# Kernel tuning notes

Hardware: AMD Instinct MI355X
Metric: run time of the kernel (lower is better)

The kernel has to match this reference:

```python
import jax, jax.numpy as jnp
import numpy as np

T, B, D_IN, UNITS = 2000, 32, 512, 1024
P_KEEP = 0.8      # eval-mode dropout mask value (1 - 0.2) for 'in', 'recur', 'orig'
BN_EPS = 1e-5     # torch BatchNorm1d default eps


def setup_inputs() -> dict:
    key = jax.random.key(0)
    ks = jax.random.split(key, 6)
    s_in = 1.0 / np.sqrt(D_IN)
    s_h = 1.0 / np.sqrt(UNITS)
    # orthogonal init for recurrent mats (as in ligru_orthinit)
    uh = jnp.linalg.qr(jax.random.normal(ks[2], (UNITS, UNITS)))[0].astype(jnp.float32)
    uz = jnp.linalg.qr(jax.random.normal(ks[3], (UNITS, UNITS)))[0].astype(jnp.float32)
    return {
        "x": jax.random.normal(ks[0], (T, B, D_IN), dtype=jnp.float32),
        "Wh": jax.random.uniform(ks[1], (UNITS, D_IN), jnp.float32, -s_in, s_in),
        "Wz": jax.random.uniform(ks[4], (UNITS, D_IN), jnp.float32, -s_in, s_in),
        "Uh": uh,
        "Uz": uz,
        "gamma_wh": jnp.ones((UNITS,), jnp.float32),
        "beta_wh": jnp.zeros((UNITS,), jnp.float32),
        "gamma_wz": jnp.ones((UNITS,), jnp.float32),
        "beta_wz": jnp.zeros((UNITS,), jnp.float32),
    }


def _batchnorm(y, gamma, beta):
    # BatchNorm1d over flattened (T*B, UNITS), biased variance (training-style stats)
    yf = y.reshape(-1, y.shape[-1])
    mean = yf.mean(axis=0)
    var = yf.var(axis=0)
    return (y - mean) * jax.lax.rsqrt(var + BN_EPS) * gamma + beta


def reference(x, Wh, Wz, Uh, Uz, gamma_wh, beta_wh, gamma_wz, beta_wz):
    # input dropout (eval mode -> constant scale 0.8) then linear, no bias (BN on)
    xd = x * P_KEEP
    wh_out = _batchnorm(jnp.einsum("tbd,ud->tbu", xd, Wh), gamma_wh, beta_wh)
    wz_out = _batchnorm(jnp.einsum("tbd,ud->tbu", xd, Wz), gamma_wz, beta_wz)

    h0 = jnp.zeros((x.shape[1], Wh.shape[0]), x.dtype)

    def step(h, inp):
        whk, wzk = inp
        z = jax.nn.sigmoid(wzk + (h * P_KEEP) @ Uz.T)   # update gate
        a = whk + (h * P_KEEP) @ Uh.T                   # candidate pre-activation
        hcand = jax.nn.relu(a) * P_KEEP                 # 'orig' dropout scale
        h_new = z * h + (1.0 - z) * hcand
        return h_new, h_new

    _, hs = jax.lax.scan(step, h0, (wh_out, wz_out))    # hs: [T, B, UNITS]
    return hs
```

## Files before the change

### kernel.cpp

```cpp
#include <hip/hip_runtime.h>


#define T_STEPS 2000
#define NCOLS   2048
#define PKEEP   0.8f
#define BN_EPSF 1e-5f
#define NW      256

typedef __attribute__((ext_vector_type(8))) short bf16x8;
typedef __attribute__((ext_vector_type(4))) float f32x4;
typedef __attribute__((ext_vector_type(4))) unsigned int u32x4;

static __device__ __forceinline__ unsigned short f2bf(float f) {
  unsigned u = __builtin_bit_cast(unsigned, f);
  unsigned r = u + 0x7FFFu + ((u >> 16) & 1u);
  return (unsigned short)(r >> 16);
}
static __device__ __forceinline__ float bf2f(unsigned short s) {
  unsigned u = ((unsigned)s) << 16;
  return __builtin_bit_cast(float, u);
}

__global__ void k_convw(const float* __restrict__ Wh, const float* __restrict__ Wz,
                        unsigned short* __restrict__ Wb) {
  int i = blockIdx.x * 256 + threadIdx.x;
  int e = i * 4;
  int n = e >> 9;
  int k = e & 511;
  const float* src = (n < 1024) ? (Wh + (size_t)n * 512 + k)
                                : (Wz + (size_t)(n - 1024) * 512 + k);
  float4 v = *(const float4*)src;
  *(ushort4*)(Wb + e) = make_ushort4(f2bf(v.x), f2bf(v.y), f2bf(v.z), f2bf(v.w));
}

__global__ __launch_bounds__(256, 2) void k_gemm(
    const float* __restrict__ X, const unsigned short* __restrict__ Wb,
    unsigned short* __restrict__ P, float* __restrict__ sums, float* __restrict__ sumsq) {
  __shared__ __align__(16) unsigned short As[128 * 32];
  __shared__ __align__(16) unsigned short Bs[128 * 32];
  const int tid  = threadIdx.x;
  const int bm   = blockIdx.x >> 4, bn = blockIdx.x & 15;
  const int lane = tid & 63, wid = tid >> 6;
  const int wm   = wid >> 1, wn = wid & 1;
  const int lrow = lane & 15, lk = lane >> 4;

  f32x4 acc[4][4] = {};

  for (int kk = 0; kk < 512; kk += 32) {
    __syncthreads();
#pragma unroll
    for (int j = 0; j < 2; ++j) {
      int c = j * 256 + wid * 64 + lane;
      int brow = c >> 2, b8 = (c & 3) * 8;
      const unsigned short* gp = Wb + (size_t)(bn * 128 + brow) * 512 + kk + b8;
      __builtin_amdgcn_global_load_lds(
          (const __attribute__((address_space(1))) unsigned int*)gp,
          (__attribute__((address_space(3))) unsigned int*)(Bs + (size_t)(j * 256 + wid * 64) * 8),
          16, 0, 0);
    }
    {
      int arow = tid >> 1, ahalf = tid & 1;
      const float4* xp = (const float4*)(X + (size_t)(bm * 128 + arow) * 512 + kk + ahalf * 16);
      unsigned v[8];
#pragma unroll
      for (int j = 0; j < 4; ++j) {
        float4 f = xp[j];
        v[j * 2 + 0] = (unsigned)f2bf(f.x) | ((unsigned)f2bf(f.y) << 16);
        v[j * 2 + 1] = (unsigned)f2bf(f.z) | ((unsigned)f2bf(f.w) << 16);
      }
      u32x4* ap = (u32x4*)(As + arow * 32 + ahalf * 16);
      u32x4 t0 = {v[0], v[1], v[2], v[3]};
      u32x4 t1 = {v[4], v[5], v[6], v[7]};
      ap[0] = t0; ap[1] = t1;
    }
    __syncthreads();

    bf16x8 af[4], bfr[4];
#pragma unroll
    for (int mt = 0; mt < 4; ++mt)
      af[mt] = *(const bf16x8*)(As + (wm * 64 + mt * 16 + lrow) * 32 + lk * 8);
#pragma unroll
    for (int nt = 0; nt < 4; ++nt)
      bfr[nt] = *(const bf16x8*)(Bs + (wn * 64 + nt * 16 + lrow) * 32 + lk * 8);
#pragma unroll
    for (int mt = 0; mt < 4; ++mt)
#pragma unroll
      for (int nt = 0; nt < 4; ++nt)
        acc[mt][nt] = __builtin_amdgcn_mfma_f32_16x16x32_bf16(af[mt], bfr[nt], acc[mt][nt], 0, 0, 0);
  }

#pragma unroll
  for (int mt = 0; mt < 4; ++mt)
#pragma unroll
    for (int nt = 0; nt < 4; ++nt) {
      f32x4 a = acc[mt][nt];
      int gcol  = bn * 128 + wn * 64 + nt * 16 + lrow;
      int grow0 = bm * 128 + wm * 64 + mt * 16 + lk * 4;
#pragma unroll
      for (int rr = 0; rr < 4; ++rr)
        P[(size_t)(grow0 + rr) * NCOLS + gcol] = f2bf(a[rr]);
    }
#pragma unroll
  for (int nt = 0; nt < 4; ++nt) {
    float s = 0.f, q = 0.f;
#pragma unroll
    for (int mt = 0; mt < 4; ++mt) {
      f32x4 a = acc[mt][nt];
#pragma unroll
      for (int rr = 0; rr < 4; ++rr) { s += a[rr]; q += a[rr] * a[rr]; }
    }
    s += __shfl_xor(s, 16); s += __shfl_xor(s, 32);
    q += __shfl_xor(q, 16); q += __shfl_xor(q, 32);
    if (lane < 16) {
      int gcol = bn * 128 + wn * 64 + nt * 16 + lrow;
      atomicAdd(&sums[gcol], s);
      atomicAdd(&sumsq[gcol], q);
    }
  }
}

__global__ __launch_bounds__(256, 1) void k_scan(
    const float* __restrict__ Uh, const float* __restrict__ Uz,
    const float* __restrict__ gwh, const float* __restrict__ bwh,
    const float* __restrict__ gwz, const float* __restrict__ bwz,
    const unsigned short* P,
    const float* __restrict__ sums, const float* __restrict__ sumsq,
    unsigned long long* hrec,
    unsigned int* ctrl,
    float* out)
{
  __shared__ __align__(16) unsigned char hlds[16384];

  const int tid  = threadIdx.x;
  const int lane = tid & 63;
  const int wid  = tid >> 6;
  const int lrow = lane & 15, lk = lane >> 4;

  const int g    = blockIdx.x & 7;
  const int role = blockIdx.x >> 3;
  const int b0   = g * 4;
  const int u0w  = role * 32 + wid * 8;
  const bool isH = (lrow >= 8);
  const int unit = u0w + (lrow & 7);
  const int col  = isH ? unit : (1024 + unit);

  float scl, bia;
  {
    float s = sums[col], q = sumsq[col];
    float gam = isH ? gwh[unit] : gwz[unit];
    float bet = isH ? bwh[unit] : bwz[unit];
    float mean = s * (1.0f / 64000.0f);
    float var  = q * (1.0f / 64000.0f) - mean * mean;
    float rstd = rsqrtf(var + BN_EPSF);
    scl = gam * rstd;
    bia = bet - mean * scl;
  }

  const float* urow = (isH ? Uh : Uz) + (size_t)unit * 1024;
  bf16x8 bfrag[32];
#pragma unroll
  for (int kt = 0; kt < 32; ++kt) {
    const float4* p4 = (const float4*)(urow + kt * 32 + lk * 8);
    float4 fa = p4[0], fb = p4[1];
    bf16x8 tv;
    tv[0] = (short)f2bf(fa.x * PKEEP); tv[1] = (short)f2bf(fa.y * PKEEP);
    tv[2] = (short)f2bf(fa.z * PKEEP); tv[3] = (short)f2bf(fa.w * PKEEP);
    tv[4] = (short)f2bf(fb.x * PKEEP); tv[5] = (short)f2bf(fb.y * PKEEP);
    tv[6] = (short)f2bf(fb.z * PKEEP); tv[7] = (short)f2bf(fb.w * PKEEP);
    bfrag[kt] = tv;
  }

  unsigned short pf[4], pn1[4];
#pragma unroll
  for (int rr = 0; rr < 4; ++rr) {
    pf[rr]  = P[(size_t)(b0 + rr) * NCOLS + col];
    pn1[rr] = P[(size_t)(32 + b0 + rr) * NCOLS + col];
  }
  __syncthreads();

  if (tid == 0) {
    __hip_atomic_fetch_add(&ctrl[0], 1u, __ATOMIC_RELEASE, __HIP_MEMORY_SCOPE_SYSTEM);
    while (__hip_atomic_load(&ctrl[0], __ATOMIC_RELAXED, __HIP_MEMORY_SCOPE_SYSTEM) < NW)
      __builtin_amdgcn_s_sleep(8);
  }
  __syncthreads();

  f32x4 hown = {0.f, 0.f, 0.f, 0.f};

  for (int t = 0; t < T_STEPS; ++t) {
    const int par = t & 1;

    const unsigned long long* rb = hrec + (((size_t)(g * 2 + par)) << 11) + tid;
    unsigned long long rec[8];
#pragma unroll
    for (int j = 0; j < 8; ++j)
      rec[j] = __hip_atomic_load(rb + 256 * j, __ATOMIC_RELAXED, __HIP_MEMORY_SCOPE_SYSTEM);
    while (true) {
      unsigned bad = 0;
#pragma unroll
      for (int j = 0; j < 8; ++j)
        if ((unsigned)(rec[j] >> 32) < (unsigned)t) bad |= (1u << j);
      if (!bad) break;
      __builtin_amdgcn_s_sleep(1);
#pragma unroll
      for (int j = 0; j < 8; ++j)
        if (bad & (1u << j))
          rec[j] = __hip_atomic_load(rb + 256 * j, __ATOMIC_RELAXED, __HIP_MEMORY_SCOPE_SYSTEM);
    }
    asm volatile("s_waitcnt vmcnt(0)" ::: "memory");

    unsigned short pn2[4] = {0, 0, 0, 0};
    if (t + 2 < T_STEPS) {
#pragma unroll
      for (int rr = 0; rr < 4; ++rr)
        pn2[rr] = P[(size_t)((t + 2) * 32 + b0 + rr) * NCOLS + col];
    }

    unsigned char* hb = hlds + par * 8192;
#pragma unroll
    for (int j = 0; j < 8; ++j) {
      int idx = tid + 256 * j;
      int row = idx >> 9, up = idx & 511;
      int byteoff = (row * 2048 + up * 4) ^ ((row & 3) << 5);
      *(unsigned*)(hb + byteoff) = (unsigned)rec[j];
    }
    asm volatile("s_waitcnt lgkmcnt(0)" ::: "memory");
    __builtin_amdgcn_sched_barrier(0);
    __builtin_amdgcn_s_barrier();
    __builtin_amdgcn_sched_barrier(0);

    f32x4 ac0 = {0.f, 0.f, 0.f, 0.f}, ac1 = ac0, ac2 = ac0, ac3 = ac0;
#pragma unroll
    for (int kt = 0; kt < 32; ++kt) {
      int ab = ((lane & 3) * 2048 + kt * 64 + lk * 16) ^ ((lane & 3) << 5);
      bf16x8 af = *(const bf16x8*)(hb + ab);
      if ((kt & 3) == 0)      ac0 = __builtin_amdgcn_mfma_f32_16x16x32_bf16(af, bfrag[kt], ac0, 0, 0, 0);
      else if ((kt & 3) == 1) ac1 = __builtin_amdgcn_mfma_f32_16x16x32_bf16(af, bfrag[kt], ac1, 0, 0, 0);
      else if ((kt & 3) == 2) ac2 = __builtin_amdgcn_mfma_f32_16x16x32_bf16(af, bfrag[kt], ac2, 0, 0, 0);
      else                    ac3 = __builtin_amdgcn_mfma_f32_16x16x32_bf16(af, bfrag[kt], ac3, 0, 0, 0);
    }
    f32x4 dsum = (ac0 + ac1) + (ac2 + ac3);

    float pre[4], oth[4];
#pragma unroll
    for (int rr = 0; rr < 4; ++rr) {
      pre[rr] = dsum[rr] + bf2f(pf[rr]) * scl + bia;
      oth[rr] = __shfl_xor(pre[rr], 8);
    }

    if (lk == 0 && isH) {
      float hn[4];
#pragma unroll
      for (int rr = 0; rr < 4; ++rr) {
        float zz = 1.0f / (1.0f + __expf(-oth[rr]));
        float hc = fmaxf(pre[rr], 0.0f) * PKEEP;
        hn[rr] = zz * hown[rr] + (1.0f - zz) * hc;
        hown[rr] = hn[rr];
      }
      float pp[4];
#pragma unroll
      for (int rr = 0; rr < 4; ++rr) pp[rr] = __shfl_xor(hn[rr], 1);
      if ((lane & 1) == 0) {
        unsigned long long* hbn = hrec + (((size_t)(g * 2 + ((t + 1) & 1))) << 11)
                                + (unit >> 1);
        unsigned tagw = (unsigned)(t + 1);
#pragma unroll
        for (int rr = 0; rr < 4; ++rr) {
          unsigned long long rcd = ((unsigned long long)tagw << 32)
                                 | (unsigned)f2bf(hn[rr]) | ((unsigned)f2bf(pp[rr]) << 16);
          __hip_atomic_store(hbn + rr * 512, rcd,
                             __ATOMIC_RELAXED, __HIP_MEMORY_SCOPE_SYSTEM);
        }
#pragma unroll
        for (int rr = 0; rr < 4; ++rr) {
          float2 ov = {hn[rr], pp[rr]};
          *(float2*)(out + (size_t)(t * 32 + b0 + rr) * 1024 + unit) = ov;
        }
      }
    }

#pragma unroll
    for (int rr = 0; rr < 4; ++rr) { pf[rr] = pn1[rr]; pn1[rr] = pn2[rr]; }
  }
}

extern "C" void kernel_launch(void* const* d_in, const int* in_sizes, int n_in,
                              void* d_out, int out_size, void* d_ws, size_t ws_size,
                              hipStream_t stream) {
  (void)in_sizes; (void)n_in; (void)out_size; (void)ws_size;
  const float* x   = (const float*)d_in[0];
  const float* Wh  = (const float*)d_in[1];
  const float* Wz  = (const float*)d_in[2];
  const float* Uh  = (const float*)d_in[3];
  const float* Uz  = (const float*)d_in[4];
  const float* gwh = (const float*)d_in[5];
  const float* bwh = (const float*)d_in[6];
  const float* gwz = (const float*)d_in[7];
  const float* bwz = (const float*)d_in[8];

  char* ws = (char*)d_ws;
  float*              sums  = (float*)(ws + 0);
  float*              sumsq = (float*)(ws + 8192);
  unsigned long long* hrec  = (unsigned long long*)(ws + 16384);
  unsigned int*       ctrl  = (unsigned int*)(ws + 278528);
  unsigned short*     Wb    = (unsigned short*)(ws + 278784);

  hipMemsetAsync(d_ws, 0, 278784, stream);
  k_convw<<<1024, 256, 0, stream>>>(Wh, Wz, Wb);
  k_gemm<<<8000, 256, 0, stream>>>(x, Wb, (unsigned short*)d_out, sums, sumsq);
  k_scan<<<NW, 256, 0, stream>>>(Uh, Uz, gwh, bwh, gwz, bwz,
                                 (const unsigned short*)d_out, sums, sumsq,
                                 hrec, ctrl, (float*)d_out);
}
```

Measured before the change: 7.818 ms.

## Halve scan workgroups to 512 threads and add per-wave tag flags for step sync

The persistent scan kernel now runs as 128 workgroups of 512 threads instead of 256 of 256, so each workgroup covers 64 units per batch group. Cross-workgroup readiness is now checked through a small per-wave tag array: one wave polls 128 tags and the workgroup barriers before loading the tagged h records. Each wave publishes its tag after its stores drain. The goal is to cut the number of polling agents and the contention on the global h records each step. The cost is an extra barrier and tag round-trip per step, plus more register pressure from the 512-thread launch bounds.

Result: slower. 8.926 ms (+14.2%).

```diff
diff --git a/kernel.cpp b/kernel.cpp
--- a/kernel.cpp
+++ b/kernel.cpp
@@ -5,7 +5,7 @@
 #define NCOLS   2048
 #define PKEEP   0.8f
 #define BN_EPSF 1e-5f
-#define NW      256
+#define NWG     128
 
 typedef __attribute__((ext_vector_type(8))) short bf16x8;
 typedef __attribute__((ext_vector_type(4))) float f32x4;
@@ -119,13 +119,14 @@
   }
 }
 
-__global__ __launch_bounds__(256, 1) void k_scan(
+__global__ __launch_bounds__(512, 2) void k_scan(
     const float* __restrict__ Uh, const float* __restrict__ Uz,
     const float* __restrict__ gwh, const float* __restrict__ bwh,
     const float* __restrict__ gwz, const float* __restrict__ bwz,
     const unsigned short* P,
     const float* __restrict__ sums, const float* __restrict__ sumsq,
     unsigned long long* hrec,
+    unsigned int* tags,
     unsigned int* ctrl,
     float* out)
 {
@@ -139,7 +140,7 @@
   const int g    = blockIdx.x & 7;
   const int role = blockIdx.x >> 3;
   const int b0   = g * 4;
-  const int u0w  = role * 32 + wid * 8;
+  const int u0w  = role * 64 + wid * 8;
   const bool isH = (lrow >= 8);
   const int unit = u0w + (lrow & 7);
   const int col  = isH ? unit : (1024 + unit);
@@ -180,7 +181,7 @@
 
   if (tid == 0) {
     __hip_atomic_fetch_add(&ctrl[0], 1u, __ATOMIC_RELEASE, __HIP_MEMORY_SCOPE_SYSTEM);
-    while (__hip_atomic_load(&ctrl[0], __ATOMIC_RELAXED, __HIP_MEMORY_SCOPE_SYSTEM) < NW)
+    while (__hip_atomic_load(&ctrl[0], __ATOMIC_RELAXED, __HIP_MEMORY_SCOPE_SYSTEM) < NWG)
       __builtin_amdgcn_s_sleep(8);
   }
   __syncthreads();
@@ -190,36 +191,51 @@
   for (int t = 0; t < T_STEPS; ++t) {
     const int par = t & 1;
 
+    unsigned short pn2[4] = {0, 0, 0, 0};
+    if (t + 2 < T_STEPS) {
+#pragma unroll
+      for (int rr = 0; rr < 4; ++rr)
+        pn2[rr] = P[(size_t)((t + 2) * 32 + b0 + rr) * NCOLS + col];
+    }
+
+    if (wid == 0) {
+      const unsigned* tg = tags + (((size_t)(g * 2 + par)) << 7);
+      unsigned ta = __hip_atomic_load(tg + lane, __ATOMIC_RELAXED, __HIP_MEMORY_SCOPE_SYSTEM);
+      unsigned tb = __hip_atomic_load(tg + 64 + lane, __ATOMIC_RELAXED, __HIP_MEMORY_SCOPE_SYSTEM);
+      while (!__all((ta >= (unsigned)t) && (tb >= (unsigned)t))) {
+        __builtin_amdgcn_s_sleep(1);
+        if (ta < (unsigned)t)
+          ta = __hip_atomic_load(tg + lane, __ATOMIC_RELAXED, __HIP_MEMORY_SCOPE_SYSTEM);
+        if (tb < (unsigned)t)
+          tb = __hip_atomic_load(tg + 64 + lane, __ATOMIC_RELAXED, __HIP_MEMORY_SCOPE_SYSTEM);
+      }
+    }
+    asm volatile("" ::: "memory");
+    __builtin_amdgcn_s_barrier();
+    asm volatile("" ::: "memory");
+
     const unsigned long long* rb = hrec + (((size_t)(g * 2 + par)) << 11) + tid;
-    unsigned long long rec[8];
-#pragma unroll
-    for (int j = 0; j < 8; ++j)
-      rec[j] = __hip_atomic_load(rb + 256 * j, __ATOMIC_RELAXED, __HIP_MEMORY_SCOPE_SYSTEM);
+    unsigned long long rec[4];
+#pragma unroll
+    for (int j = 0; j < 4; ++j)
+      rec[j] = __hip_atomic_load(rb + 512 * j, __ATOMIC_RELAXED, __HIP_MEMORY_SCOPE_SYSTEM);
     while (true) {
       unsigned bad = 0;
 #pragma unroll
-      for (int j = 0; j < 8; ++j)
+      for (int j = 0; j < 4; ++j)
         if ((unsigned)(rec[j] >> 32) < (unsigned)t) bad |= (1u << j);
       if (!bad) break;
       __builtin_amdgcn_s_sleep(1);
 #pragma unroll
-      for (int j = 0; j < 8; ++j)
+      for (int j = 0; j < 4; ++j)
         if (bad & (1u << j))
-          rec[j] = __hip_atomic_load(rb + 256 * j, __ATOMIC_RELAXED, __HIP_MEMORY_SCOPE_SYSTEM);
-    }
-    asm volatile("s_waitcnt vmcnt(0)" ::: "memory");
-
-    unsigned short pn2[4] = {0, 0, 0, 0};
-    if (t + 2 < T_STEPS) {
-#pragma unroll
-      for (int rr = 0; rr < 4; ++rr)
-        pn2[rr] = P[(size_t)((t + 2) * 32 + b0 + rr) * NCOLS + col];
+          rec[j] = __hip_atomic_load(rb + 512 * j, __ATOMIC_RELAXED, __HIP_MEMORY_SCOPE_SYSTEM);
     }
 
     unsigned char* hb = hlds + par * 8192;
 #pragma unroll
-    for (int j = 0; j < 8; ++j) {
-      int idx = tid + 256 * j;
+    for (int j = 0; j < 4; ++j) {
+      int idx = tid + 512 * j;
       int row = idx >> 9, up = idx & 511;
       int byteoff = (row * 2048 + up * 4) ^ ((row & 3) << 5);
       *(unsigned*)(hb + byteoff) = (unsigned)rec[j];
@@ -277,6 +293,13 @@
           *(float2*)(out + (size_t)(t * 32 + b0 + rr) * 1024 + unit) = ov;
         }
       }
+    }
+
+    asm volatile("s_waitcnt vmcnt(0)" ::: "memory");
+    __builtin_amdgcn_sched_barrier(0);
+    if (lane == 8) {
+      __hip_atomic_store(tags + (((size_t)(g * 2 + ((t + 1) & 1))) << 7) + (role * 8 + wid),
+                         (unsigned)(t + 1), __ATOMIC_RELAXED, __HIP_MEMORY_SCOPE_SYSTEM);
     }
 
 #pragma unroll
@@ -302,13 +325,14 @@
   float*              sums  = (float*)(ws + 0);
   float*              sumsq = (float*)(ws + 8192);
   unsigned long long* hrec  = (unsigned long long*)(ws + 16384);
-  unsigned int*       ctrl  = (unsigned int*)(ws + 278528);
-  unsigned short*     Wb    = (unsigned short*)(ws + 278784);
-
-  hipMemsetAsync(d_ws, 0, 278784, stream);
+  unsigned int*       tags  = (unsigned int*)(ws + 278528);
+  unsigned int*       ctrl  = (unsigned int*)(ws + 286720);
+  unsigned short*     Wb    = (unsigned short*)(ws + 286848);
+
+  hipMemsetAsync(d_ws, 0, 286848, stream);
   k_convw<<<1024, 256, 0, stream>>>(Wh, Wz, Wb);
   k_gemm<<<8000, 256, 0, stream>>>(x, Wb, (unsigned short*)d_out, sums, sumsq);
-  k_scan<<<NW, 256, 0, stream>>>(Uh, Uz, gwh, bwh, gwz, bwz,
-                                 (const unsigned short*)d_out, sums, sumsq,
-                                 hrec, ctrl, (float*)d_out);
-}
+  k_scan<<<NWG, 512, 0, stream>>>(Uh, Uz, gwh, bwh, gwz, bwz,
+                                  (const unsigned short*)d_out, sums, sumsq,
+                                  hrec, tags, ctrl, (float*)d_out);
+}
```

## Halve scan workgroups, each interleaving two batch groups to overlap sync waits

Applied to the files above, without the earlier changes.

The recurrent scan kernel now launches 128 workgroups instead of 256. Each one keeps the same U weight fragments in registers and processes two batch groups per time step. Group B's hidden-state records are loaded and polled while group A's MFMA and gate math run, so some of the cross-workgroup synchronization latency is hidden behind compute. The cost is twice the serial compute per workgroup per step and half the CUs left idle.

Measured after the change: 8.031 ms. 1.03x slower.

```diff
diff --git a/kernel.cpp b/kernel.cpp
--- a/kernel.cpp
+++ b/kernel.cpp
@@ -5,7 +5,7 @@
 #define NCOLS   2048
 #define PKEEP   0.8f
 #define BN_EPSF 1e-5f
-#define NW      256
+#define NWG     128
 
 typedef __attribute__((ext_vector_type(8))) short bf16x8;
 typedef __attribute__((ext_vector_type(4))) float f32x4;
@@ -129,16 +129,17 @@
     unsigned int* ctrl,
     float* out)
 {
-  __shared__ __align__(16) unsigned char hlds[16384];
+  __shared__ __align__(16) unsigned char hlds[4][8192];
 
   const int tid  = threadIdx.x;
   const int lane = tid & 63;
   const int wid  = tid >> 6;
   const int lrow = lane & 15, lk = lane >> 4;
 
-  const int g    = blockIdx.x & 7;
-  const int role = blockIdx.x >> 3;
-  const int b0   = g * 4;
+  const int pair = blockIdx.x & 3;
+  const int role = blockIdx.x >> 2;
+  const int gA   = pair * 2, gB = pair * 2 + 1;
+  const int b0A  = gA * 4,   b0B = gB * 4;
   const int u0w  = role * 32 + wid * 8;
   const bool isH = (lrow >= 8);
   const int unit = u0w + (lrow & 7);
@@ -170,117 +171,213 @@
     bfrag[kt] = tv;
   }
 
-  unsigned short pf[4], pn1[4];
+  unsigned short pfA[4], pn1A[4], pfB[4], pn1B[4];
 #pragma unroll
   for (int rr = 0; rr < 4; ++rr) {
-    pf[rr]  = P[(size_t)(b0 + rr) * NCOLS + col];
-    pn1[rr] = P[(size_t)(32 + b0 + rr) * NCOLS + col];
+    pfA[rr]  = P[(size_t)(b0A + rr) * NCOLS + col];
+    pn1A[rr] = P[(size_t)(32 + b0A + rr) * NCOLS + col];
+    pfB[rr]  = P[(size_t)(b0B + rr) * NCOLS + col];
+    pn1B[rr] = P[(size_t)(32 + b0B + rr) * NCOLS + col];
   }
   __syncthreads();
 
   if (tid == 0) {
     __hip_atomic_fetch_add(&ctrl[0], 1u, __ATOMIC_RELEASE, __HIP_MEMORY_SCOPE_SYSTEM);
-    while (__hip_atomic_load(&ctrl[0], __ATOMIC_RELAXED, __HIP_MEMORY_SCOPE_SYSTEM) < NW)
+    while (__hip_atomic_load(&ctrl[0], __ATOMIC_RELAXED, __HIP_MEMORY_SCOPE_SYSTEM) < NWG)
       __builtin_amdgcn_s_sleep(8);
   }
   __syncthreads();
 
-  f32x4 hown = {0.f, 0.f, 0.f, 0.f};
+  float hownA[4] = {0.f, 0.f, 0.f, 0.f};
+  float hownB[4] = {0.f, 0.f, 0.f, 0.f};
 
   for (int t = 0; t < T_STEPS; ++t) {
-    const int par = t & 1;
-
-    const unsigned long long* rb = hrec + (((size_t)(g * 2 + par)) << 11) + tid;
-    unsigned long long rec[8];
+    const int par  = t & 1;
+    const int npar = (t + 1) & 1;
+    const unsigned tagw = (unsigned)(t + 1);
+
+    const unsigned long long* rbA = hrec + (((size_t)(gA * 2 + par)) << 11) + tid;
+    unsigned long long recA[8];
 #pragma unroll
     for (int j = 0; j < 8; ++j)
-      rec[j] = __hip_atomic_load(rb + 256 * j, __ATOMIC_RELAXED, __HIP_MEMORY_SCOPE_SYSTEM);
+      recA[j] = __hip_atomic_load(rbA + 256 * j, __ATOMIC_RELAXED, __HIP_MEMORY_SCOPE_SYSTEM);
     while (true) {
       unsigned bad = 0;
 #pragma unroll
       for (int j = 0; j < 8; ++j)
-        if ((unsigned)(rec[j] >> 32) < (unsigned)t) bad |= (1u << j);
+        if ((unsigned)(recA[j] >> 32) < (unsigned)t) bad |= (1u << j);
       if (!bad) break;
       __builtin_amdgcn_s_sleep(1);
 #pragma unroll
       for (int j = 0; j < 8; ++j)
         if (bad & (1u << j))
-          rec[j] = __hip_atomic_load(rb + 256 * j, __ATOMIC_RELAXED, __HIP_MEMORY_SCOPE_SYSTEM);
+          recA[j] = __hip_atomic_load(rbA + 256 * j, __ATOMIC_RELAXED, __HIP_MEMORY_SCOPE_SYSTEM);
     }
     asm volatile("s_waitcnt vmcnt(0)" ::: "memory");
 
-    unsigned short pn2[4] = {0, 0, 0, 0};
+    unsigned short pn2A[4] = {0, 0, 0, 0}, pn2B[4] = {0, 0, 0, 0};
     if (t + 2 < T_STEPS) {
 #pragma unroll
-      for (int rr = 0; rr < 4; ++rr)
-        pn2[rr] = P[(size_t)((t + 2) * 32 + b0 + rr) * NCOLS + col];
-    }
-
-    unsigned char* hb = hlds + par * 8192;
-#pragma unroll
-    for (int j = 0; j < 8; ++j) {
-      int idx = tid + 256 * j;
-      int row = idx >> 9, up = idx & 511;
-      int byteoff = (row * 2048 + up * 4) ^ ((row & 3) << 5);
-      *(unsigned*)(hb + byteoff) = (unsigned)rec[j];
+      for (int rr = 0; rr < 4; ++rr) {
+        pn2A[rr] = P[(size_t)((t + 2) * 32 + b0A + rr) * NCOLS + col];
+        pn2B[rr] = P[(size_t)((t + 2) * 32 + b0B + rr) * NCOLS + col];
+      }
+    }
+
+    {
+      unsigned char* hb = hlds[par];
+#pragma unroll
+      for (int j = 0; j < 8; ++j) {
+        int idx = tid + 256 * j;
+        int row = idx >> 9, up = idx & 511;
+        int byteoff = (row * 2048 + up * 4) ^ ((row & 3) << 5);
+        *(unsigned*)(hb + byteoff) = (unsigned)recA[j];
+      }
     }
     asm volatile("s_waitcnt lgkmcnt(0)" ::: "memory");
     __builtin_amdgcn_sched_barrier(0);
     __builtin_amdgcn_s_barrier();
     __builtin_amdgcn_sched_barrier(0);
 
-    f32x4 ac0 = {0.f, 0.f, 0.f, 0.f}, ac1 = ac0, ac2 = ac0, ac3 = ac0;
-#pragma unroll
-    for (int kt = 0; kt < 32; ++kt) {
-      int ab = ((lane & 3) * 2048 + kt * 64 + lk * 16) ^ ((lane & 3) << 5);
-      bf16x8 af = *(const bf16x8*)(hb + ab);
-      if ((kt & 3) == 0)      ac0 = __builtin_amdgcn_mfma_f32_16x16x32_bf16(af, bfrag[kt], ac0, 0, 0, 0);
-      else if ((kt & 3) == 1) ac1 = __builtin_amdgcn_mfma_f32_16x16x32_bf16(af, bfrag[kt], ac1, 0, 0, 0);
-      else if ((kt & 3) == 2) ac2 = __builtin_amdgcn_mfma_f32_16x16x32_bf16(af, bfrag[kt], ac2, 0, 0, 0);
-      else                    ac3 = __builtin_amdgcn_mfma_f32_16x16x32_bf16(af, bfrag[kt], ac3, 0, 0, 0);
-    }
-    f32x4 dsum = (ac0 + ac1) + (ac2 + ac3);
-
-    float pre[4], oth[4];
+    const unsigned long long* rbB = hrec + (((size_t)(gB * 2 + par)) << 11) + tid;
+    unsigned long long recB[8];
+#pragma unroll
+    for (int j = 0; j < 8; ++j)
+      recB[j] = __hip_atomic_load(rbB + 256 * j, __ATOMIC_RELAXED, __HIP_MEMORY_SCOPE_SYSTEM);
+
+    {
+      unsigned char* hb = hlds[par];
+      f32x4 ac0 = {0.f, 0.f, 0.f, 0.f}, ac1 = ac0, ac2 = ac0, ac3 = ac0;
+#pragma unroll
+      for (int kt = 0; kt < 32; ++kt) {
+        int ab = ((lane & 3) * 2048 + kt * 64 + lk * 16) ^ ((lane & 3) << 5);
+        bf16x8 af = *(const bf16x8*)(hb + ab);
+        if ((kt & 3) == 0)      ac0 = __builtin_amdgcn_mfma_f32_16x16x32_bf16(af, bfrag[kt], ac0, 0, 0, 0);
+        else if ((kt & 3) == 1) ac1 = __builtin_amdgcn_mfma_f32_16x16x32_bf16(af, bfrag[kt], ac1, 0, 0, 0);
+        else if ((kt & 3) == 2) ac2 = __builtin_amdgcn_mfma_f32_16x16x32_bf16(af, bfrag[kt], ac2, 0, 0, 0);
+        else                    ac3 = __builtin_amdgcn_mfma_f32_16x16x32_bf16(af, bfrag[kt], ac3, 0, 0, 0);
+      }
+      f32x4 dsum = (ac0 + ac1) + (ac2 + ac3);
+
+      float pre[4], oth[4];
+#pragma unroll
+      for (int rr = 0; rr < 4; ++rr) {
+        pre[rr] = dsum[rr] + bf2f(pfA[rr]) * scl + bia;
+        oth[rr] = __shfl_xor(pre[rr], 8);
+      }
+      if (lk == 0 && isH) {
+        float hn[4];
+#pragma unroll
+        for (int rr = 0; rr < 4; ++rr) {
+          float zz = 1.0f / (1.0f + __expf(-oth[rr]));
+          float hc = fmaxf(pre[rr], 0.0f) * PKEEP;
+          hn[rr] = zz * hownA[rr] + (1.0f - zz) * hc;
+          hownA[rr] = hn[rr];
+        }
+        float pp[4];
+#pragma unroll
+        for (int rr = 0; rr < 4; ++rr) pp[rr] = __shfl_xor(hn[rr], 1);
+        if ((lane & 1) == 0) {
+          unsigned long long* hbn = hrec + (((size_t)(gA * 2 + npar)) << 11) + (unit >> 1);
+#pragma unroll
+          for (int rr = 0; rr < 4; ++rr) {
+            unsigned long long rcd = ((unsigned long long)tagw << 32)
+                                   | (unsigned)f2bf(hn[rr]) | ((unsigned)f2bf(pp[rr]) << 16);
+            __hip_atomic_store(hbn + rr * 512, rcd,
+                               __ATOMIC_RELAXED, __HIP_MEMORY_SCOPE_SYSTEM);
+          }
+#pragma unroll
+          for (int rr = 0; rr < 4; ++rr) {
+            float2 ov = {hn[rr], pp[rr]};
+            *(float2*)(out + (size_t)(t * 32 + b0A + rr) * 1024 + unit) = ov;
+          }
+        }
+      }
+    }
+
+    while (true) {
+      unsigned bad = 0;
+#pragma unroll
+      for (int j = 0; j < 8; ++j)
+        if ((unsigned)(recB[j] >> 32) < (unsigned)t) bad |= (1u << j);
+      if (!bad) break;
+      __builtin_amdgcn_s_sleep(1);
+#pragma unroll
+      for (int j = 0; j < 8; ++j)
+        if (bad & (1u << j))
+          recB[j] = __hip_atomic_load(rbB + 256 * j, __ATOMIC_RELAXED, __HIP_MEMORY_SCOPE_SYSTEM);
+    }
+
+    {
+      unsigned char* hb = hlds[2 + par];
+#pragma unroll
+      for (int j = 0; j < 8; ++j) {
+        int idx = tid + 256 * j;
+        int row = idx >> 9, up = idx & 511;
+        int byteoff = (row * 2048 + up * 4) ^ ((row & 3) << 5);
+        *(unsigned*)(hb + byteoff) = (unsigned)recB[j];
+      }
+    }
+    asm volatile("s_waitcnt lgkmcnt(0)" ::: "memory");
+    __builtin_amdgcn_sched_barrier(0);
+    __builtin_amdgcn_s_barrier();
+    __builtin_amdgcn_sched_barrier(0);
+
+    {
+      unsigned char* hb = hlds[2 + par];
+      f32x4 ac0 = {0.f, 0.f, 0.f, 0.f}, ac1 = ac0, ac2 = ac0, ac3 = ac0;
+#pragma unroll
+      for (int kt = 0; kt < 32; ++kt) {
+        int ab = ((lane & 3) * 2048 + kt * 64 + lk * 16) ^ ((lane & 3) << 5);
+        bf16x8 af = *(const bf16x8*)(hb + ab);
+        if ((kt & 3) == 0)      ac0 = __builtin_amdgcn_mfma_f32_16x16x32_bf16(af, bfrag[kt], ac0, 0, 0, 0);
+        else if ((kt & 3) == 1) ac1 = __builtin_amdgcn_mfma_f32_16x16x32_bf16(af, bfrag[kt], ac1, 0, 0, 0);
+        else if ((kt & 3) == 2) ac2 = __builtin_amdgcn_mfma_f32_16x16x32_bf16(af, bfrag[kt], ac2, 0, 0, 0);
+        else                    ac3 = __builtin_amdgcn_mfma_f32_16x16x32_bf16(af, bfrag[kt], ac3, 0, 0, 0);
+      }
+      f32x4 dsum = (ac0 + ac1) + (ac2 + ac3);
+
+      float pre[4], oth[4];
+#pragma unroll
+      for (int rr = 0; rr < 4; ++rr) {
+        pre[rr] = dsum[rr] + bf2f(pfB[rr]) * scl + bia;
+        oth[rr] = __shfl_xor(pre[rr], 8);
+      }
+      if (lk == 0 && isH) {
+        float hn[4];
+#pragma unroll
+        for (int rr = 0; rr < 4; ++rr) {
+          float zz = 1.0f / (1.0f + __expf(-oth[rr]));
+          float hc = fmaxf(pre[rr], 0.0f) * PKEEP;
+          hn[rr] = zz * hownB[rr] + (1.0f - zz) * hc;
+          hownB[rr] = hn[rr];
+        }
+        float pp[4];
+#pragma unroll
+        for (int rr = 0; rr < 4; ++rr) pp[rr] = __shfl_xor(hn[rr], 1);
+        if ((lane & 1) == 0) {
+          unsigned long long* hbn = hrec + (((size_t)(gB * 2 + npar)) << 11) + (unit >> 1);
+#pragma unroll
+          for (int rr = 0; rr < 4; ++rr) {
+            unsigned long long rcd = ((unsigned long long)tagw << 32)
+                                   | (unsigned)f2bf(hn[rr]) | ((unsigned)f2bf(pp[rr]) << 16);
+            __hip_atomic_store(hbn + rr * 512, rcd,
+                               __ATOMIC_RELAXED, __HIP_MEMORY_SCOPE_SYSTEM);
+          }
+#pragma unroll
+          for (int rr = 0; rr < 4; ++rr) {
+            float2 ov = {hn[rr], pp[rr]};
+            *(float2*)(out + (size_t)(t * 32 + b0B + rr) * 1024 + unit) = ov;
+          }
+        }
+      }
+    }
+
 #pragma unroll
     for (int rr = 0; rr < 4; ++rr) {
-      pre[rr] = dsum[rr] + bf2f(pf[rr]) * scl + bia;
-      oth[rr] = __shfl_xor(pre[rr], 8);
-    }
-
-    if (lk == 0 && isH) {
-      float hn[4];
-#pragma unroll
-      for (int rr = 0; rr < 4; ++rr) {
-        float zz = 1.0f / (1.0f + __expf(-oth[rr]));
-        float hc = fmaxf(pre[rr], 0.0f) * PKEEP;
-        hn[rr] = zz * hown[rr] + (1.0f - zz) * hc;
-        hown[rr] = hn[rr];
-      }
-      float pp[4];
-#pragma unroll
-      for (int rr = 0; rr < 4; ++rr) pp[rr] = __shfl_xor(hn[rr], 1);
-      if ((lane & 1) == 0) {
-        unsigned long long* hbn = hrec + (((size_t)(g * 2 + ((t + 1) & 1))) << 11)
-                                + (unit >> 1);
-        unsigned tagw = (unsigned)(t + 1);
-#pragma unroll
-        for (int rr = 0; rr < 4; ++rr) {
-          unsigned long long rcd = ((unsigned long long)tagw << 32)
-                                 | (unsigned)f2bf(hn[rr]) | ((unsigned)f2bf(pp[rr]) << 16);
-          __hip_atomic_store(hbn + rr * 512, rcd,
-                             __ATOMIC_RELAXED, __HIP_MEMORY_SCOPE_SYSTEM);
-        }
-#pragma unroll
-        for (int rr = 0; rr < 4; ++rr) {
-          float2 ov = {hn[rr], pp[rr]};
-          *(float2*)(out + (size_t)(t * 32 + b0 + rr) * 1024 + unit) = ov;
-        }
-      }
-    }
-
-#pragma unroll
-    for (int rr = 0; rr < 4; ++rr) { pf[rr] = pn1[rr]; pn1[rr] = pn2[rr]; }
+      pfA[rr] = pn1A[rr]; pn1A[rr] = pn2A[rr];
+      pfB[rr] = pn1B[rr]; pn1B[rr] = pn2B[rr];
+    }
   }
 }
 
@@ -308,7 +405,7 @@
   hipMemsetAsync(d_ws, 0, 278784, stream);
   k_convw<<<1024, 256, 0, stream>>>(Wh, Wz, Wb);
   k_gemm<<<8000, 256, 0, stream>>>(x, Wb, (unsigned short*)d_out, sums, sumsq);
-  k_scan<<<NW, 256, 0, stream>>>(Uh, Uz, gwh, bwh, gwz, bwz,
-                                 (const unsigned short*)d_out, sums, sumsq,
-                                 hrec, ctrl, (float*)d_out);
-}
+  k_scan<<<NWG, 256, 0, stream>>>(Uh, Uz, gwh, bwh, gwz, bwz,
+                                  (const unsigned short*)d_out, sums, sumsq,
+                                  hrec, ctrl, (float*)d_out);
+}
```

## Replace per-step block barrier with per-chunk LDS flags for streaming h consumption

Applied to the files above, without the earlier changes.

Each step used to wait until the whole hidden-state record set for the group had arrived, then pass a workgroup barrier before any MFMA ran. Now each wave polls its own 64-record chunks, writes each one to LDS as soon as it is tagged, and raises a per-chunk LDS flag. The MFMA loop spins on each chunk's flag, so the matmul can start on partial data instead of waiting for the slowest producer. The global record layout is changed so each producer block writes a contiguous 64-record chunk, and an LDS counter guards reuse of the double buffer. The cost is extra spin-waits on LDS atomics and more complex ordering, which risks ordering bugs or contention.

Result: slower. 13.89 ms (+77.7%).

```diff
diff --git a/kernel.cpp b/kernel.cpp
--- a/kernel.cpp
+++ b/kernel.cpp
@@ -5,7 +5,7 @@
 #define NCOLS   2048
 #define PKEEP   0.8f
 #define BN_EPSF 1e-5f
-#define NW      256
+#define NWG     256
 
 typedef __attribute__((ext_vector_type(8))) short bf16x8;
 typedef __attribute__((ext_vector_type(4))) float f32x4;
@@ -129,7 +129,9 @@
     unsigned int* ctrl,
     float* out)
 {
-  __shared__ __align__(16) unsigned char hlds[16384];
+  __shared__ __align__(16) unsigned char hlds[2][8192];
+  __shared__ unsigned int lflag[2][32];
+  __shared__ unsigned int lcnt[2];
 
   const int tid  = threadIdx.x;
   const int lane = tid & 63;
@@ -143,6 +145,9 @@
   const bool isH = (lrow >= 8);
   const int unit = u0w + (lrow & 7);
   const int col  = isH ? unit : (1024 + unit);
+
+  if (tid < 32) { lflag[0][tid] = 0u; lflag[1][tid] = 0u; }
+  if (tid < 2)  { lcnt[tid] = 0u; }
 
   float scl, bia;
   {
@@ -180,34 +185,16 @@
 
   if (tid == 0) {
     __hip_atomic_fetch_add(&ctrl[0], 1u, __ATOMIC_RELEASE, __HIP_MEMORY_SCOPE_SYSTEM);
-    while (__hip_atomic_load(&ctrl[0], __ATOMIC_RELAXED, __HIP_MEMORY_SCOPE_SYSTEM) < NW)
+    while (__hip_atomic_load(&ctrl[0], __ATOMIC_RELAXED, __HIP_MEMORY_SCOPE_SYSTEM) < NWG)
       __builtin_amdgcn_s_sleep(8);
   }
   __syncthreads();
 
-  f32x4 hown = {0.f, 0.f, 0.f, 0.f};
+  float hown[4] = {0.f, 0.f, 0.f, 0.f};
 
   for (int t = 0; t < T_STEPS; ++t) {
-    const int par = t & 1;
-
-    const unsigned long long* rb = hrec + (((size_t)(g * 2 + par)) << 11) + tid;
-    unsigned long long rec[8];
-#pragma unroll
-    for (int j = 0; j < 8; ++j)
-      rec[j] = __hip_atomic_load(rb + 256 * j, __ATOMIC_RELAXED, __HIP_MEMORY_SCOPE_SYSTEM);
-    while (true) {
-      unsigned bad = 0;
-#pragma unroll
-      for (int j = 0; j < 8; ++j)
-        if ((unsigned)(rec[j] >> 32) < (unsigned)t) bad |= (1u << j);
-      if (!bad) break;
-      __builtin_amdgcn_s_sleep(1);
-#pragma unroll
-      for (int j = 0; j < 8; ++j)
-        if (bad & (1u << j))
-          rec[j] = __hip_atomic_load(rb + 256 * j, __ATOMIC_RELAXED, __HIP_MEMORY_SCOPE_SYSTEM);
-    }
-    asm volatile("s_waitcnt vmcnt(0)" ::: "memory");
+    const int par  = t & 1;
+    const int npar = (t + 1) & 1;
 
     unsigned short pn2[4] = {0, 0, 0, 0};
     if (t + 2 < T_STEPS) {
@@ -216,29 +203,58 @@
         pn2[rr] = P[(size_t)((t + 2) * 32 + b0 + rr) * NCOLS + col];
     }
 
-    unsigned char* hb = hlds + par * 8192;
-#pragma unroll
-    for (int j = 0; j < 8; ++j) {
-      int idx = tid + 256 * j;
-      int row = idx >> 9, up = idx & 511;
-      int byteoff = (row * 2048 + up * 4) ^ ((row & 3) << 5);
-      *(unsigned*)(hb + byteoff) = (unsigned)rec[j];
-    }
-    asm volatile("s_waitcnt lgkmcnt(0)" ::: "memory");
-    __builtin_amdgcn_sched_barrier(0);
-    __builtin_amdgcn_s_barrier();
-    __builtin_amdgcn_sched_barrier(0);
+    const unsigned long long* rb = hrec + (((size_t)(g * 2 + par)) << 11);
+    unsigned long long rec[8];
+#pragma unroll
+    for (int i = 0; i < 8; ++i)
+      rec[i] = __hip_atomic_load(rb + (wid + i * 4) * 64 + lane,
+                                 __ATOMIC_RELAXED, __HIP_MEMORY_SCOPE_SYSTEM);
+
+    if (t >= 2) {
+      unsigned need = 4u * (unsigned)(t >> 1);
+      while (__hip_atomic_load(&lcnt[par], __ATOMIC_ACQUIRE,
+                               __HIP_MEMORY_SCOPE_WORKGROUP) < need)
+        __builtin_amdgcn_s_sleep(1);
+    }
+
+    {
+      unsigned done = 0;
+      while (done != 0xFFu) {
+#pragma unroll
+        for (int i = 0; i < 8; ++i) {
+          if (done & (1u << i)) continue;
+          if (__all((int)((unsigned)(rec[i] >> 32) >= (unsigned)t))) {
+            int c = wid + i * 4;
+            int row = lane >> 4;
+            int boff = (row * 2048 + c * 64 + (lane & 15) * 4) ^ ((row & 3) << 5);
+            *(unsigned*)(hlds[par] + boff) = (unsigned)rec[i];
+            __hip_atomic_store(&lflag[par][c], (unsigned)(t + 1),
+                               __ATOMIC_RELEASE, __HIP_MEMORY_SCOPE_WORKGROUP);
+            done |= (1u << i);
+          } else {
+            rec[i] = __hip_atomic_load(rb + (wid + i * 4) * 64 + lane,
+                                       __ATOMIC_RELAXED, __HIP_MEMORY_SCOPE_SYSTEM);
+          }
+        }
+        if (done != 0xFFu) __builtin_amdgcn_s_sleep(1);
+      }
+    }
 
     f32x4 ac0 = {0.f, 0.f, 0.f, 0.f}, ac1 = ac0, ac2 = ac0, ac3 = ac0;
 #pragma unroll
-    for (int kt = 0; kt < 32; ++kt) {
-      int ab = ((lane & 3) * 2048 + kt * 64 + lk * 16) ^ ((lane & 3) << 5);
-      bf16x8 af = *(const bf16x8*)(hb + ab);
-      if ((kt & 3) == 0)      ac0 = __builtin_amdgcn_mfma_f32_16x16x32_bf16(af, bfrag[kt], ac0, 0, 0, 0);
-      else if ((kt & 3) == 1) ac1 = __builtin_amdgcn_mfma_f32_16x16x32_bf16(af, bfrag[kt], ac1, 0, 0, 0);
-      else if ((kt & 3) == 2) ac2 = __builtin_amdgcn_mfma_f32_16x16x32_bf16(af, bfrag[kt], ac2, 0, 0, 0);
-      else                    ac3 = __builtin_amdgcn_mfma_f32_16x16x32_bf16(af, bfrag[kt], ac3, 0, 0, 0);
-    }
+    for (int c = 0; c < 32; ++c) {
+      while (__hip_atomic_load(&lflag[par][c], __ATOMIC_ACQUIRE,
+                               __HIP_MEMORY_SCOPE_WORKGROUP) < (unsigned)(t + 1)) { }
+      int ab = ((lane & 3) * 2048 + c * 64 + lk * 16) ^ ((lane & 3) << 5);
+      bf16x8 af = *(const bf16x8*)(hlds[par] + ab);
+      if ((c & 3) == 0)      ac0 = __builtin_amdgcn_mfma_f32_16x16x32_bf16(af, bfrag[c], ac0, 0, 0, 0);
+      else if ((c & 3) == 1) ac1 = __builtin_amdgcn_mfma_f32_16x16x32_bf16(af, bfrag[c], ac1, 0, 0, 0);
+      else if ((c & 3) == 2) ac2 = __builtin_amdgcn_mfma_f32_16x16x32_bf16(af, bfrag[c], ac2, 0, 0, 0);
+      else                   ac3 = __builtin_amdgcn_mfma_f32_16x16x32_bf16(af, bfrag[c], ac3, 0, 0, 0);
+    }
+    if (lane == 0)
+      __hip_atomic_fetch_add(&lcnt[par], 1u, __ATOMIC_RELEASE, __HIP_MEMORY_SCOPE_WORKGROUP);
+
     f32x4 dsum = (ac0 + ac1) + (ac2 + ac3);
 
     float pre[4], oth[4];
@@ -261,14 +277,16 @@
 #pragma unroll
       for (int rr = 0; rr < 4; ++rr) pp[rr] = __shfl_xor(hn[rr], 1);
       if ((lane & 1) == 0) {
-        unsigned long long* hbn = hrec + (((size_t)(g * 2 + ((t + 1) & 1))) << 11)
-                                + (unit >> 1);
+        asm volatile("s_waitcnt vmcnt(0)" ::: "memory");
+        int pairIdx = wid * 4 + ((lane - 8) >> 1);
+        unsigned long long* hbn = hrec + (((size_t)(g * 2 + npar)) << 11)
+                                + role * 64 + pairIdx;
         unsigned tagw = (unsigned)(t + 1);
 #pragma unroll
         for (int rr = 0; rr < 4; ++rr) {
           unsigned long long rcd = ((unsigned long long)tagw << 32)
                                  | (unsigned)f2bf(hn[rr]) | ((unsigned)f2bf(pp[rr]) << 16);
-          __hip_atomic_store(hbn + rr * 512, rcd,
+          __hip_atomic_store(hbn + rr * 16, rcd,
                              __ATOMIC_RELAXED, __HIP_MEMORY_SCOPE_SYSTEM);
         }
 #pragma unroll
@@ -308,7 +326,7 @@
   hipMemsetAsync(d_ws, 0, 278784, stream);
   k_convw<<<1024, 256, 0, stream>>>(Wh, Wz, Wb);
   k_gemm<<<8000, 256, 0, stream>>>(x, Wb, (unsigned short*)d_out, sums, sumsq);
-  k_scan<<<NW, 256, 0, stream>>>(Uh, Uz, gwh, bwh, gwz, bwz,
-                                 (const unsigned short*)d_out, sums, sumsq,
-                                 hrec, ctrl, (float*)d_out);
-}
+  k_scan<<<NWG, 256, 0, stream>>>(Uh, Uz, gwh, bwh, gwz, bwz,
+                                  (const unsigned short*)d_out, sums, sumsq,
+                                  hrec, ctrl, (float*)d_out);
+}
```
